# Kernel tuning notes

Hardware: AMD Instinct MI355X
Metric: run time of the kernel (lower is better)

Reference implementation:

```python
import jax, jax.numpy as jnp
import numpy as np

N, M, NTYPES, C, AXIS = 4096, 128, 2, 64, 16
TYPE_IDX = (0, 2048, 4096)        # atom-type partition along center axis
NTYPE_IDX = (0, 64, 128)          # neighbor-type partition along neighbor axis
RCUT = 6.0
BOX = 20.0
SR_MEAN = (0.1, 0.1)              # precomputed stats (get_stats)
SR_STD = (0.05, 0.05)
NORM = 20.0                       # avg neighbor count + 1


def setup_inputs() -> dict:
    key = jax.random.key(0)
    ks = jax.random.split(key, 16)
    coord_3N = jax.random.uniform(ks[0], (3, N), dtype=jnp.float32) * BOX
    box = jnp.full((3,), BOX, dtype=jnp.float32)
    # neighbors sorted by type: first 64 of type 0, last 64 of type 1
    nbr0 = jax.random.randint(ks[1], (N, M // 2), 0, TYPE_IDX[1])
    nbr1 = jax.random.randint(ks[2], (N, M // 2), TYPE_IDX[1], TYPE_IDX[2])
    nbrs_idx = jnp.concatenate([nbr0, nbr1], axis=1).astype(jnp.int32)
    # 4 per-(center,neighbor)-type embedding nets, widths 1->16->32->64, stacked
    eW0 = jax.random.normal(ks[3], (4, 1, 16), dtype=jnp.float32)
    eb0 = jax.random.normal(ks[4], (4, 16), dtype=jnp.float32) * 0.1
    eW1 = jax.random.normal(ks[5], (4, 16, 32), dtype=jnp.float32) / 4.0
    eb1 = jax.random.normal(ks[6], (4, 32), dtype=jnp.float32) * 0.1
    eW2 = jax.random.normal(ks[7], (4, 32, 64), dtype=jnp.float32) / (32.0 ** 0.5)
    eb2 = jax.random.normal(ks[8], (4, 64), dtype=jnp.float32) * 0.1
    Tbias = jnp.zeros((1, C), dtype=jnp.float32)
    # 2 per-type fitting nets, widths 1024->128->128->1, stacked
    fW0 = jax.random.normal(ks[9], (2, AXIS * C, 128), dtype=jnp.float32) / (AXIS * C) ** 0.5
    fb0 = jnp.zeros((2, 128), dtype=jnp.float32)
    fW1 = jax.random.normal(ks[10], (2, 128, 128), dtype=jnp.float32) / (128.0 ** 0.5)
    fb1 = jnp.zeros((2, 128), dtype=jnp.float32)
    fW2 = jax.random.normal(ks[11], (2, 128, 1), dtype=jnp.float32) / (128.0 ** 0.5)
    fb2 = jnp.zeros((2, 1), dtype=jnp.float32)
    Ebias = jnp.zeros((2,), dtype=jnp.float32)
    return {"coord_3N": coord_3N, "box": box, "nbrs_idx": nbrs_idx,
            "eW0": eW0, "eb0": eb0, "eW1": eW1, "eb1": eb1, "eW2": eW2, "eb2": eb2,
            "Tbias": Tbias, "fW0": fW0, "fb0": fb0, "fW1": fW1, "fb1": fb1,
            "fW2": fW2, "fb2": fb2, "Ebias": Ebias}


def reference(coord_3N, box, nbrs_idx, eW0, eb0, eW1, eb1, eW2, eb2,
              Tbias, fW0, fb0, fW1, fb1, fW2, fb2, Ebias):
    # --- neighbor gather + minimal-image relative coords (get_relative_coord) ---
    x_3NM = coord_3N[:, nbrs_idx] - coord_3N[:, :, None]            # [3,N,M]
    x_3NM = x_3NM - box[:, None, None] * jnp.round(x_3NM / box[:, None, None])
    r2 = (x_3NM ** 2).sum(0)
    mask = r2 > 1e-12
    rsafe = jnp.sqrt(jnp.where(mask, r2, 1.0))                      # safe for grads
    r_NM = jnp.where(mask, rsafe, 0.0)                              # [N,M]
    # --- smooth radial feature sr(r) = switch(r)/r ---
    sw = 0.5 * jnp.cos(jnp.pi * jnp.minimum(r_NM, RCUT) / RCUT) + 0.5
    sr_NM = jnp.where(mask & (r_NM < RCUT), sw / rsafe, 0.0)
    # --- per-center-type normalization (slice_t / concat_t over type_idx) ---
    srn_rows, srcn = [], []
    for i in range(NTYPES):
        blk = sr_NM[TYPE_IDX[i]:TYPE_IDX[i + 1]]
        srn_rows.append(blk / SR_STD[i])
        srcn.append((blk - SR_MEAN[i]) / SR_STD[i])
    sr_norm_NM = jnp.concatenate(srn_rows, 0)
    x_norm_3NM = x_3NM / jnp.where(mask, rsafe, 1.0)[None]
    R_3NM = 3 ** 0.5 * sr_norm_NM * x_norm_3NM
    R2diag_3NM = 9 ** 0.5 * sr_norm_NM * (x_norm_3NM ** 2 - 1.0 / 3.0)
    R2offd_3NM = 18 ** 0.5 * sr_norm_NM * (x_norm_3NM * jnp.stack([x_norm_3NM[1], x_norm_3NM[2], x_norm_3NM[0]]))
    R_XNM = jnp.concatenate([sr_norm_NM[None], R_3NM, R2diag_3NM, R2offd_3NM])  # [10,N,M]

    # --- per-(center,neighbor)-type embedding MLPs on scalar sr feature ---
    def embed(x, k):  # x: [n, m] -> [n, m, C]
        h = jnp.tanh(x[:, :, None] @ eW0[k] + eb0[k])
        h = jnp.tanh(h @ eW1[k] + eb1[k])
        return jnp.tanh(h @ eW2[k] + eb2[k])

    rows = []
    for i in range(NTYPES):
        cols = [embed(srcn[i][:, NTYPE_IDX[j]:NTYPE_IDX[j + 1]], i * NTYPES + j)
                for j in range(NTYPES)]
        rows.append(jnp.concatenate(cols, 1))
    embed_NMC = jnp.concatenate(rows, 0)                            # [N,M,C]

    # --- descriptor contraction ---
    T_NXC = jnp.einsum('xnm,nmc->nxc', R_XNM, embed_NMC) / NORM     # [N,10,C]
    T_NC = T_NXC[:, 0] + Tbias
    T_N3C = T_NXC[:, 1:4]
    T_N6C = T_NXC[:, 4:]
    G_NAC = T_NC[:, None] * T_NC[:, :AXIS, None] \
        + (T_N3C[:, :, None] * T_N3C[:, :, :AXIS, None]).sum(1)     # [N,AXIS,C]
    # use_2nd branch
    G1 = T_N3C[:, :, AXIS:2 * AXIS]                                 # [N,3,AXIS]
    G11 = jnp.concatenate([G1 ** 2,
                           2 ** 0.5 * G1 * jnp.stack([G1[:, 1], G1[:, 2], G1[:, 0]], axis=1)], axis=1)
    G2 = G11 + T_N6C[:, :, AXIS:2 * AXIS]                           # [N,6,AXIS]
    G_NAC = G_NAC + jnp.einsum('nxa,nxc->nac', G2, T_N6C)

    # --- per-type fitting nets ---
    Gflat = G_NAC.reshape(N, AXIS * C)
    energy = jnp.zeros((), dtype=Gflat.dtype)
    for t in range(NTYPES):
        g = Gflat[TYPE_IDX[t]:TYPE_IDX[t + 1]]
        h = jnp.tanh(g @ fW0[t] + fb0[t])
        h = jnp.tanh(h @ fW1[t] + fb1[t])
        f = h @ fW2[t] + fb2[t]
        energy = energy + (f + Ebias[t]).sum()
    return energy
```

## Files before the change

### kernel.cpp

```cpp
#include <hip/hip_runtime.h>
#include <hip/hip_fp16.h>

typedef _Float16 h16;
typedef h16 v2h __attribute__((ext_vector_type(2)));
typedef h16 v4h __attribute__((ext_vector_type(4)));
typedef h16 v8h __attribute__((ext_vector_type(8)));
typedef float f4 __attribute__((ext_vector_type(4)));

#define NATOM 4096
#define HALF_N 2048
#define K2 2.885390081777927f
#define GSCL 0.015625f
#define W0SCL (64.0f * K2)
#define USCL 0.0625f
#define GOUTS (GSCL / USCL)

#define TBL_N 2048
#define W0MIN_ (-0.201f)
#define DW_ (1.2005f / 2047.0f)
#define RSCALE_ (2047.0f / 1.2005f)

__device__ __forceinline__ float rcp_fast(float x) {
#if __has_builtin(__builtin_amdgcn_rcpf)
  return __builtin_amdgcn_rcpf(x);
#else
  return 1.0f / x;
#endif
}

__device__ __forceinline__ float exp2_fast(float x) {
#if __has_builtin(__builtin_amdgcn_exp2f)
  return __builtin_amdgcn_exp2f(x);
#else
  return exp2f(x);
#endif
}

__device__ __forceinline__ float tanh_e2(float d) {
  float r = rcp_fast(1.0f + exp2_fast(d));
  return fmaf(-2.0f, r, 1.0f);
}

__device__ __forceinline__ v8h lds_v8h(const h16* base, int byte) {
  return *(const v8h*)((const char*)base + byte);
}

__global__ __launch_bounds__(256) void k_setup(
    const float* __restrict__ eW0, const float* __restrict__ eb0,
    const float* __restrict__ eW1, const float* __restrict__ eb1,
    const float* __restrict__ eW2, const float* __restrict__ eb2,
    const float* __restrict__ fW0, const float* __restrict__ fW1,
    const float* __restrict__ coord,
    h16* __restrict__ tbl, h16* __restrict__ W0t, h16* __restrict__ W1t,
    f4* __restrict__ coordP)
{
  const int bid = blockIdx.x, tid = threadIdx.x;
  if (bid < 512) {
    __shared__ float sW1[512];
    __shared__ float sW2[2048];
    __shared__ float sW0s[16], sb0s[16], sb1s[32], sb2s[64];
    const int net = bid >> 7;
    for (int i = tid; i < 512; i += 256) sW1[i] = eW1[net * 512 + i];
    for (int i = tid; i < 2048; i += 256) sW2[i] = eW2[net * 2048 + i];
    if (tid < 16) { sW0s[tid] = eW0[net * 16 + tid]; sb0s[tid] = eb0[net * 16 + tid]; }
    else if (tid >= 32 && tid < 64) sb1s[tid - 32] = eb1[net * 32 + tid - 32];
    else if (tid >= 64 && tid < 128) sb2s[tid - 64] = eb2[net * 64 + tid - 64];
    __syncthreads();

    const int u = (bid & 127) * 256 + tid;
    const int e = u >> 4, cq = u & 15;
    const float w = W0MIN_ + (float)e * DW_;
    const float s = 8.0f * w * rcp_fast(1.0f - fabsf(w));
    float h0[16];
#pragma unroll
    for (int i = 0; i < 16; ++i)
      h0[i] = tanh_e2(K2 * fmaf(s, sW0s[i], sb0s[i]));
    float h1[32];
#pragma unroll
    for (int j = 0; j < 32; ++j) {
      float a = sb1s[j];
#pragma unroll
      for (int i = 0; i < 16; ++i) a = fmaf(h0[i], sW1[i * 32 + j], a);
      h1[j] = tanh_e2(K2 * a);
    }
    f4 a4 = *(const f4*)&sb2s[cq * 4];
    for (int j = 0; j < 32; ++j) {
      f4 wv4 = *(const f4*)&sW2[j * 64 + cq * 4];
      a4 += h1[j] * wv4;
    }
    union { h16 e4[4]; unsigned long long q; } o;
#pragma unroll
    for (int q = 0; q < 4; ++q) o.e4[q] = (h16)tanh_e2(K2 * a4[q]);
    *(unsigned long long*)&tbl[((size_t)(net * TBL_N + e)) * 64 + cq * 4] = o.q;
  } else if (bid < 640) {
    int idx = (bid - 512) * 256 + tid;
    int t = idx >> 14, n = idx & 127, k8 = (idx >> 7) & 127;
    union { v8h v; h16 e[8]; } o;
#pragma unroll
    for (int i = 0; i < 8; ++i)
      o.e[i] = (h16)(W0SCL * fW0[(size_t)t * 131072 + (size_t)(k8 * 8 + i) * 128 + n]);
    *(v8h*)&W0t[((size_t)t * 128 + n) * 1024 + k8 * 8] = o.v;
  } else if (bid < 656) {
    int idx = (bid - 640) * 256 + tid;
    f4 c;
    c.x = coord[idx]; c.y = coord[NATOM + idx]; c.z = coord[2 * NATOM + idx];
    c.w = 0.0f;
    coordP[idx] = c;
  } else {
    int idx = (bid - 656) * 256 + tid;
    int t = idx >> 11, rem = idx & 2047;
    int n = rem >> 4, k8 = rem & 15;
    union { v8h v; h16 e[8]; } o;
#pragma unroll
    for (int i = 0; i < 8; ++i)
      o.e[i] = (h16)(K2 * fW1[(size_t)t * 16384 + (size_t)(k8 * 8 + i) * 128 + n]);
    *(v8h*)&W1t[((size_t)t * 128 + n) * 128 + k8 * 8] = o.v;
  }
}

__global__ __launch_bounds__(256, 4) void k_embed(
    const f4* __restrict__ coordP, const float* __restrict__ box,
    const int* __restrict__ nbrs, const float* __restrict__ Tbias,
    const h16* __restrict__ tbl, h16* __restrict__ Gout)
{
  __shared__ h16 pool1[4][2560] __attribute__((aligned(16)));
  __shared__ h16 pool2[4][1360] __attribute__((aligned(16)));

  const int tid = threadIdx.x;
  const int wv = tid >> 6;
  const int lane = tid & 63;
  const int n = blockIdx.x * 4 + wv;
  const int ti = (n >= HALF_N) ? 1 : 0;
  const int c15 = lane & 15, g4 = lane >> 4;
  const int mp = lane >> 2, cg = lane & 3;

  h16* E32 = &pool1[wv][0];
  h16* Rl  = &pool2[wv][0];

  const int jnb0 = nbrs[(size_t)n * 128 + lane];
  const int jnb1 = nbrs[(size_t)n * 128 + 64 + lane];

  int uf0 = 0, uf1 = 0;
  {
    const float bx = box[0], by = box[1], bz = box[2];
    const float rbx = rcp_fast(bx), rby = rcp_fast(by), rbz = rcp_fast(bz);
    const f4 cme = coordP[n];
#pragma unroll
    for (int nb = 0; nb < 2; ++nb) {
      const int m = nb * 64 + lane;
      const f4 cj = coordP[nb ? jnb1 : jnb0];
      float dx = cj.x - cme.x;
      float dy = cj.y - cme.y;
      float dz = cj.z - cme.z;
      dx -= bx * rintf(dx * rbx);
      dy -= by * rintf(dy * rby);
      dz -= bz * rintf(dz * rbz);
      float r2 = dx * dx + dy * dy + dz * dz;
      bool mk = r2 > 1e-12f;
      float rs = sqrtf(mk ? r2 : 1.0f);
      float r  = mk ? rs : 0.0f;
      float sw = 0.5f * __cosf(0.52359878f * fminf(r, 6.0f)) + 0.5f;
      float invr = mk ? rcp_fast(rs) : 1.0f;
      float sr = (mk && r < 6.0f) ? sw * invr : 0.0f;
      float x0 = dx * invr, x1 = dy * invr, x2 = dz * invr;
      float srn = sr * 20.0f;
      float s   = (sr - 0.1f) * 20.0f;
      Rl[0 * 136 + m] = (h16)srn;
      Rl[1 * 136 + m] = (h16)(1.7320508f * srn * x0);
      Rl[2 * 136 + m] = (h16)(1.7320508f * srn * x1);
      Rl[3 * 136 + m] = (h16)(1.7320508f * srn * x2);
      Rl[4 * 136 + m] = (h16)(3.0f * srn * (x0 * x0 - 0.33333334f));
      Rl[5 * 136 + m] = (h16)(3.0f * srn * (x1 * x1 - 0.33333334f));
      Rl[6 * 136 + m] = (h16)(3.0f * srn * (x2 * x2 - 0.33333334f));
      Rl[7 * 136 + m] = (h16)(4.2426407f * srn * (x0 * x1));
      Rl[8 * 136 + m] = (h16)(4.2426407f * srn * (x1 * x2));
      Rl[9 * 136 + m] = (h16)(4.2426407f * srn * (x2 * x0));
      float wr = s * rcp_fast(8.0f + fabsf(s));
      float fidx = (wr - W0MIN_) * RSCALE_;
      fidx = fminf(fmaxf(fidx, 0.0f), 2045.99f);
      float i0f = floorf(fidx);
      h16 frh = (h16)(fidx - i0f);
      int uf = ((int)i0f << 16) |
               (int)__builtin_bit_cast(unsigned short, frh);
      if (nb == 0) uf0 = uf; else uf1 = uf;
    }
  }

  union U8 { v8h v; v2h p[4]; h16 e[8]; };
  const int rrow = (c15 < 10) ? c15 : 9;
  const v8h vzero = {};
  f4 tac[4];
#pragma unroll
  for (int nt = 0; nt < 4; ++nt) tac[nt] = (f4){0.f, 0.f, 0.f, 0.f};

  auto issue = [&](int ks, U8* buf, float* fr) {
#pragma unroll
    for (int e = 0; e < 2; ++e) {
      int src = ((ks & 1) * 32 + mp * 2 + e) * 4;
      unsigned uu = (unsigned)__builtin_amdgcn_ds_bpermute(src, (ks < 2) ? uf0 : uf1);
      int i0 = (int)(uu >> 16);
      fr[e] = (float)__builtin_bit_cast(h16, (unsigned short)(uu & 0xffffu));
      const int net = ti * 2 + (ks >> 1);
      const h16* rp = tbl + ((size_t)net * TBL_N + i0) * 64 + cg * 16;
      buf[e * 4 + 0].v = *(const v8h*)(rp);
      buf[e * 4 + 1].v = *(const v8h*)(rp + 8);
      buf[e * 4 + 2].v = *(const v8h*)(rp + 64);
      buf[e * 4 + 3].v = *(const v8h*)(rp + 72);
    }
  };

  auto proc = [&](int ks, U8* buf, const float* fr) {
    v2h f0; f0.x = (h16)fr[0]; f0.y = (h16)fr[0];
    v2h f1; f1.x = (h16)fr[1]; f1.y = (h16)fr[1];
    const int m0 = mp * 2;
#pragma unroll
    for (int ch8 = 0; ch8 < 2; ++ch8) {
#pragma unroll
      for (int p = 0; p < 4; ++p) {
        v2h e0 = buf[ch8].p[p]     + f0 * (buf[2 + ch8].p[p] - buf[ch8].p[p]);
        v2h e1 = buf[4 + ch8].p[p] + f1 * (buf[6 + ch8].p[p] - buf[4 + ch8].p[p]);
        const int c = cg * 16 + ch8 * 8 + p * 2;
        v2h w0; w0.x = e0.x; w0.y = e1.x;
        v2h w1; w1.x = e0.y; w1.y = e1.y;
        *(v2h*)&E32[c * 40 + m0]       = w0;
        *(v2h*)&E32[(c + 1) * 40 + m0] = w1;
      }
    }
    v8h ra = *(const v8h*)&Rl[rrow * 136 + ks * 32 + g4 * 8];
    if (c15 >= 10) ra = vzero;
#pragma unroll
    for (int nt = 0; nt < 4; ++nt) {
      v8h bf = *(const v8h*)&E32[(nt * 16 + c15) * 40 + g4 * 8];
      tac[nt] = __builtin_amdgcn_mfma_f32_16x16x32_f16(ra, bf, tac[nt], 0, 0, 0);
    }
  };

  U8 bA[8], bB[8];
  float frA[2], frB[2];
  issue(0, bA, frA);
  issue(1, bB, frB);
  proc(0, bA, frA);
  issue(2, bA, frA);
  proc(1, bB, frB);
  issue(3, bB, frB);
  proc(2, bA, frA);
  proc(3, bB, frB);

  h16* Vt = E32;
  h16* Ul = Rl;
#pragma unroll
  for (int nt = 0; nt < 4; ++nt) {
    const int col = nt * 16 + c15;
    float tb = (g4 == 0) ? Tbias[col] : 0.0f;
    v4h pk;
    pk[0] = (h16)(tac[nt][0] * 0.05f + tb);
    pk[1] = (h16)(tac[nt][1] * 0.05f);
    pk[2] = (h16)(tac[nt][2] * 0.05f);
    pk[3] = (h16)(tac[nt][3] * 0.05f);
    *(v4h*)&Vt[col * 40 + g4 * 4] = pk;
  }
  *(v8h*)&Vt[lane * 40 + 16] = vzero;
  *(v8h*)&Vt[lane * 40 + 24] = vzero;

  if (lane < 16) {
    const h16* va = &Vt[lane * 40];
    const h16* vb = &Vt[(16 + lane) * 40];
    v8h Ta = *(const v8h*)va;
    v8h Tb = *(const v8h*)vb;
    v2h Tb8 = *(const v2h*)(vb + 8);
    float g1x = (float)Tb[1], g1y = (float)Tb[2], g1z = (float)Tb[3];
    v8h up;
    up[0] = (h16)((float)Ta[0] * USCL);
    up[1] = (h16)((float)Ta[1] * USCL);
    up[2] = (h16)((float)Ta[2] * USCL);
    up[3] = (h16)((float)Ta[3] * USCL);
    up[4] = (h16)((g1x * g1x + (float)Tb[4]) * USCL);
    up[5] = (h16)((g1y * g1y + (float)Tb[5]) * USCL);
    up[6] = (h16)((g1z * g1z + (float)Tb[6]) * USCL);
    up[7] = (h16)((1.4142135f * g1x * g1y + (float)Tb[7]) * USCL);
    *(v8h*)&Ul[lane * 40] = up;
    v2h u89;
    u89.x = (h16)((1.4142135f * g1y * g1z + (float)Tb8[0]) * USCL);
    u89.y = (h16)((1.4142135f * g1z * g1x + (float)Tb8[1]) * USCL);
    *(v2h*)&Ul[lane * 40 + 8] = u89;
    v2h z2 = {};
    v4h z4 = {};
    *(v2h*)&Ul[lane * 40 + 10] = z2;
    *(v4h*)&Ul[lane * 40 + 12] = z4;
    *(v8h*)&Ul[lane * 40 + 16] = vzero;
    *(v8h*)&Ul[lane * 40 + 24] = vzero;
  }

  {
    v8h ua = *(const v8h*)&Ul[c15 * 40 + g4 * 8];
    h16* gp = Gout + (size_t)n * 1024;
#pragma unroll
    for (int nt = 0; nt < 4; ++nt) {
      v8h vb = *(const v8h*)&Vt[(nt * 16 + c15) * 40 + g4 * 8];
      f4 z = (f4){0.f, 0.f, 0.f, 0.f};
      f4 g = __builtin_amdgcn_mfma_f32_16x16x32_f16(ua, vb, z, 0, 0, 0);
#pragma unroll
      for (int r = 0; r < 4; ++r) {
        const int a = g4 * 4 + r;
        gp[a * 64 + nt * 16 + c15] = (h16)(g[r] * GOUTS);
      }
    }
  }
}

__global__ __launch_bounds__(256) void k_fit(
    const h16* __restrict__ G16, const h16* __restrict__ W0t,
    const h16* __restrict__ W1t,
    const float* __restrict__ fb0, const float* __restrict__ fb1,
    const float* __restrict__ fW2, const float* __restrict__ fb2,
    const float* __restrict__ Ebias, float* __restrict__ BP)
{
  __shared__ h16 As[2][32][64]  __attribute__((aligned(16)));
  __shared__ h16 Bs[2][128][64] __attribute__((aligned(16)));
  __shared__ h16 ht[32][128]    __attribute__((aligned(16)));
  __shared__ h16 W1s[128][128]  __attribute__((aligned(16)));
  __shared__ float red[32][33];

  const int tid = threadIdx.x;
  const int abase = blockIdx.x * 32;
  const int t = (abase >= HALF_N) ? 1 : 0;
  const int lane = tid & 63, w = tid >> 6;
  const int c15 = lane & 15, g4 = lane >> 4;
  const int rt = w & 1, ng = w >> 1;

  float fb0v[4], b1v[4], w2v[4];
#pragma unroll
  for (int nt = 0; nt < 4; ++nt) {
    const int nn = ng * 64 + nt * 16 + c15;
    fb0v[nt] = K2 * fb0[t * 128 + nn];
    b1v[nt]  = K2 * fb1[t * 128 + nn];
    w2v[nt]  = fW2[t * 128 + nn];
  }

#pragma unroll
  for (int u = 0; u < 8; ++u) {
    int idx = u * 256 + tid;
    int nrow = idx >> 4, c8 = idx & 15;
    v8h v = *(const v8h*)&W1t[((size_t)t * 128 + nrow) * 128 + c8 * 8];
    int byte = nrow * 256 + ((c8 * 16) ^ ((nrow & 7) << 4));
    *(v8h*)((char*)&W1s[0][0] + byte) = v;
  }

  f4 acc[4];
#pragma unroll
  for (int nt = 0; nt < 4; ++nt) acc[nt] = (f4){0.f, 0.f, 0.f, 0.f};

  auto stageK = [&](int kc, int p) {
    {
      int r = tid >> 3, c8 = tid & 7;
      v8h v = *(const v8h*)&G16[(size_t)(abase + r) * 1024 + kc * 64 + c8 * 8];
      int byte = r * 128 + ((c8 * 16) ^ ((r & 7) << 4));
      *(v8h*)((char*)&As[p][0][0] + byte) = v;
    }
#pragma unroll
    for (int u = 0; u < 4; ++u) {
      int idx = u * 256 + tid;
      int nrow = idx >> 3, c8 = idx & 7;
      v8h v = *(const v8h*)&W0t[((size_t)t * 128 + nrow) * 1024 + kc * 64 + c8 * 8];
      int byte = nrow * 128 + ((c8 * 16) ^ ((nrow & 7) << 4));
      *(v8h*)((char*)&Bs[p][0][0] + byte) = v;
    }
  };

  stageK(0, 0);
  __syncthreads();
  for (int kc = 0; kc < 16; ++kc) {
    const int p = kc & 1;
    if (kc < 15) stageK(kc + 1, p ^ 1);
#pragma unroll
    for (int ksub = 0; ksub < 2; ++ksub) {
      const int ar = rt * 16 + c15;
      const int koff = (ksub * 32 + g4 * 8) * 2;
      v8h a = lds_v8h(&As[p][0][0], ar * 128 + (koff ^ ((ar & 7) << 4)));
#pragma unroll
      for (int nt = 0; nt < 4; ++nt) {
        const int br = ng * 64 + nt * 16 + c15;
        v8h b = lds_v8h(&Bs[p][0][0], br * 128 + (koff ^ ((br & 7) << 4)));
        acc[nt] = __builtin_amdgcn_mfma_f32_16x16x32_f16(a, b, acc[nt], 0, 0, 0);
      }
    }
    __syncthreads();
  }

#pragma unroll
  for (int nt = 0; nt < 4; ++nt)
#pragma unroll
    for (int r = 0; r < 4; ++r) {
      int a = rt * 16 + g4 * 4 + r;
      int k = ng * 64 + nt * 16 + c15;
      h16 hv = (h16)tanh_e2(acc[nt][r] + fb0v[nt]);
      int byte = a * 256 + ((k * 2) ^ ((a & 7) << 4));
      *((h16*)((char*)&ht[0][0] + byte)) = hv;
    }
  __syncthreads();

  f4 acc2[4];
#pragma unroll
  for (int nt = 0; nt < 4; ++nt) acc2[nt] = (f4){0.f, 0.f, 0.f, 0.f};
#pragma unroll
  for (int ks2 = 0; ks2 < 4; ++ks2) {
    const int ar = rt * 16 + c15;
    const int koff = (ks2 * 32 + g4 * 8) * 2;
    v8h a = lds_v8h(&ht[0][0], ar * 256 + (koff ^ ((ar & 7) << 4)));
#pragma unroll
    for (int nt = 0; nt < 4; ++nt) {
      const int br = ng * 64 + nt * 16 + c15;
      v8h b = lds_v8h(&W1s[0][0], br * 256 + (koff ^ ((br & 7) << 4)));
      acc2[nt] = __builtin_amdgcn_mfma_f32_16x16x32_f16(a, b, acc2[nt], 0, 0, 0);
    }
  }

#pragma unroll
  for (int r = 0; r < 4; ++r) {
    float v = 0.0f;
#pragma unroll
    for (int nt = 0; nt < 4; ++nt)
      v += tanh_e2(acc2[nt][r] + b1v[nt]) * w2v[nt];
    red[rt * 16 + g4 * 4 + r][ng * 16 + c15] = v;
  }
  __syncthreads();
  if (tid < 64) {
    const int a = tid & 31, half = tid >> 5;
    float s = 0.0f;
#pragma unroll
    for (int c = 0; c < 16; ++c) s += red[a][half * 16 + c];
    s += __shfl_xor(s, 32);
    s += __shfl_xor(s, 16);
    s += __shfl_xor(s, 8);
    s += __shfl_xor(s, 4);
    s += __shfl_xor(s, 2);
    s += __shfl_xor(s, 1);
    if (tid == 0) BP[blockIdx.x] = s + 32.0f * (fb2[t] + Ebias[t]);
  }
}

__global__ __launch_bounds__(64) void k_reduce(const float* __restrict__ BP,
                                               float* __restrict__ out)
{
  int tid = threadIdx.x;
  float s = BP[tid] + BP[tid + 64];
  s += __shfl_xor(s, 32);
  s += __shfl_xor(s, 16);
  s += __shfl_xor(s, 8);
  s += __shfl_xor(s, 4);
  s += __shfl_xor(s, 2);
  s += __shfl_xor(s, 1);
  if (tid == 0) out[0] = s;
}

extern "C" void kernel_launch(void* const* d_in, const int* in_sizes, int n_in,
                              void* d_out, int out_size, void* d_ws, size_t ws_size,
                              hipStream_t stream) {
  const float* coord = (const float*)d_in[0];
  const float* box   = (const float*)d_in[1];
  const int*   nbrs  = (const int*)d_in[2];
  const float* eW0   = (const float*)d_in[3];
  const float* eb0   = (const float*)d_in[4];
  const float* eW1   = (const float*)d_in[5];
  const float* eb1   = (const float*)d_in[6];
  const float* eW2   = (const float*)d_in[7];
  const float* eb2   = (const float*)d_in[8];
  const float* Tbias = (const float*)d_in[9];
  const float* fW0   = (const float*)d_in[10];
  const float* fb0   = (const float*)d_in[11];
  const float* fW1   = (const float*)d_in[12];
  const float* fb1   = (const float*)d_in[13];
  const float* fW2   = (const float*)d_in[14];
  const float* fb2   = (const float*)d_in[15];
  const float* Ebias = (const float*)d_in[16];

  char* ws = (char*)d_ws;
  h16*   G16 = (h16*)ws;
  h16*   W0t = (h16*)(ws + (size_t)8  * 1024 * 1024);
  h16*   W1t = (h16*)(ws + (size_t)9  * 1024 * 1024);
  h16*   tbl = (h16*)(ws + (size_t)10 * 1024 * 1024);
  f4*    cP  = (f4*)(ws + (size_t)11 * 1024 * 1024);
  float* BP  = (float*)(ws + (size_t)12 * 1024 * 1024);

  k_setup<<<672, 256, 0, stream>>>(eW0, eb0, eW1, eb1, eW2, eb2, fW0, fW1,
                                   coord, tbl, W0t, W1t, cP);
  k_embed<<<1024, 256, 0, stream>>>(cP, box, nbrs, Tbias, tbl, G16);
  k_fit<<<128, 256, 0, stream>>>(G16, W0t, W1t, fb0, fb1, fW2, fb2, Ebias, BP);
  k_reduce<<<1, 64, 0, stream>>>(BP, (float*)d_out);
}
```

Baseline: 42.70 us.

## Halve fit tile rows, double blocks, fuse final reduction via atomic counter

The fitting kernel now processes 16 atoms per block instead of 32, launching 256 blocks to fill more compute units, with a larger K-chunk and a single shared LDS pool reused across stages. The separate reduction kernel is removed: each block publishes its partial sum and the last block to arrive, detected via an atomic counter reset in setup, sums all partials. The setup embedding layer-1 matmul is also vectorised using a transposed weight layout. This trades duplicate weight loads per block and atomic ordering overhead for better occupancy and one fewer launch.

```diff
diff --git a/kernel.cpp b/kernel.cpp
--- a/kernel.cpp
+++ b/kernel.cpp
@@ -52,15 +52,18 @@
     const float* __restrict__ fW0, const float* __restrict__ fW1,
     const float* __restrict__ coord,
     h16* __restrict__ tbl, h16* __restrict__ W0t, h16* __restrict__ W1t,
-    f4* __restrict__ coordP)
+    f4* __restrict__ coordP, int* __restrict__ counter)
 {
   const int bid = blockIdx.x, tid = threadIdx.x;
   if (bid < 512) {
-    __shared__ float sW1[512];
+    __shared__ float sW1t[32][16];
     __shared__ float sW2[2048];
     __shared__ float sW0s[16], sb0s[16], sb1s[32], sb2s[64];
     const int net = bid >> 7;
-    for (int i = tid; i < 512; i += 256) sW1[i] = eW1[net * 512 + i];
+    for (int i = tid; i < 512; i += 256) {
+      int j = i >> 4, ii = i & 15;
+      sW1t[j][ii] = eW1[net * 512 + ii * 32 + j];
+    }
     for (int i = tid; i < 2048; i += 256) sW2[i] = eW2[net * 2048 + i];
     if (tid < 16) { sW0s[tid] = eW0[net * 16 + tid]; sb0s[tid] = eb0[net * 16 + tid]; }
     else if (tid >= 32 && tid < 64) sb1s[tid - 32] = eb1[net * 32 + tid - 32];
@@ -75,12 +78,20 @@
 #pragma unroll
     for (int i = 0; i < 16; ++i)
       h0[i] = tanh_e2(K2 * fmaf(s, sW0s[i], sb0s[i]));
+    f4 h04[4];
+#pragma unroll
+    for (int q = 0; q < 4; ++q) {
+      h04[q].x = h0[q * 4]; h04[q].y = h0[q * 4 + 1];
+      h04[q].z = h0[q * 4 + 2]; h04[q].w = h0[q * 4 + 3];
+    }
     float h1[32];
 #pragma unroll
     for (int j = 0; j < 32; ++j) {
-      float a = sb1s[j];
-#pragma unroll
-      for (int i = 0; i < 16; ++i) a = fmaf(h0[i], sW1[i * 32 + j], a);
+      f4 p = h04[0] * (*(const f4*)&sW1t[j][0]);
+      p += h04[1] * (*(const f4*)&sW1t[j][4]);
+      p += h04[2] * (*(const f4*)&sW1t[j][8]);
+      p += h04[3] * (*(const f4*)&sW1t[j][12]);
+      float a = sb1s[j] + (p.x + p.y) + (p.z + p.w);
       h1[j] = tanh_e2(K2 * a);
     }
     f4 a4 = *(const f4*)&sb2s[cq * 4];
@@ -101,6 +112,7 @@
       o.e[i] = (h16)(W0SCL * fW0[(size_t)t * 131072 + (size_t)(k8 * 8 + i) * 128 + n]);
     *(v8h*)&W0t[((size_t)t * 128 + n) * 1024 + k8 * 8] = o.v;
   } else if (bid < 656) {
+    if (bid == 640 && tid == 0) *counter = 0;
     int idx = (bid - 640) * 256 + tid;
     f4 c;
     c.x = coord[idx]; c.y = coord[NATOM + idx]; c.z = coord[2 * NATOM + idx];
@@ -308,149 +320,152 @@
   }
 }
 
-__global__ __launch_bounds__(256) void k_fit(
+__global__ __launch_bounds__(256, 2) void k_fit(
     const h16* __restrict__ G16, const h16* __restrict__ W0t,
     const h16* __restrict__ W1t,
     const float* __restrict__ fb0, const float* __restrict__ fb1,
     const float* __restrict__ fW2, const float* __restrict__ fb2,
-    const float* __restrict__ Ebias, float* __restrict__ BP)
+    const float* __restrict__ Ebias,
+    float* __restrict__ BP, int* __restrict__ counter,
+    float* __restrict__ out)
 {
-  __shared__ h16 As[2][32][64]  __attribute__((aligned(16)));
-  __shared__ h16 Bs[2][128][64] __attribute__((aligned(16)));
-  __shared__ h16 ht[32][128]    __attribute__((aligned(16)));
-  __shared__ h16 W1s[128][128]  __attribute__((aligned(16)));
-  __shared__ float red[32][33];
-
+  __shared__ h16 pool[36864] __attribute__((aligned(16)));
+  __shared__ int lastFlag;
   const int tid = threadIdx.x;
-  const int abase = blockIdx.x * 32;
+  const int abase = blockIdx.x * 16;
   const int t = (abase >= HALF_N) ? 1 : 0;
   const int lane = tid & 63, w = tid >> 6;
   const int c15 = lane & 15, g4 = lane >> 4;
-  const int rt = w & 1, ng = w >> 1;
-
-  float fb0v[4], b1v[4], w2v[4];
-#pragma unroll
-  for (int nt = 0; nt < 4; ++nt) {
-    const int nn = ng * 64 + nt * 16 + c15;
+
+  float fb0v[2], b1v[2], w2v[2];
+#pragma unroll
+  for (int nt = 0; nt < 2; ++nt) {
+    const int nn = w * 32 + nt * 16 + c15;
     fb0v[nt] = K2 * fb0[t * 128 + nn];
     b1v[nt]  = K2 * fb1[t * 128 + nn];
     w2v[nt]  = fW2[t * 128 + nn];
   }
 
+  auto stageK = [&](int kc, int p) {
+    {
+      int r = tid >> 4, c8 = tid & 15;
+      v8h v = *(const v8h*)&G16[(size_t)(abase + r) * 1024 + kc * 128 + c8 * 8];
+      int byte = p * 36864 + r * 256 + ((c8 * 16) ^ ((r & 7) << 4));
+      *(v8h*)((char*)pool + byte) = v;
+    }
+#pragma unroll
+    for (int u = 0; u < 8; ++u) {
+      int idx = u * 256 + tid;
+      int nr = idx >> 4, c8 = idx & 15;
+      v8h v = *(const v8h*)&W0t[((size_t)t * 128 + nr) * 1024 + kc * 128 + c8 * 8];
+      int byte = p * 36864 + 4096 + nr * 256 + ((c8 * 16) ^ ((nr & 7) << 4));
+      *(v8h*)((char*)pool + byte) = v;
+    }
+  };
+
+  f4 acc[2];
+  acc[0] = (f4){0.f, 0.f, 0.f, 0.f};
+  acc[1] = (f4){0.f, 0.f, 0.f, 0.f};
+
+  stageK(0, 0);
+  __syncthreads();
+  for (int kc = 0; kc < 8; ++kc) {
+    const int p = kc & 1;
+    if (kc < 7) stageK(kc + 1, p ^ 1);
+#pragma unroll
+    for (int ksub = 0; ksub < 4; ++ksub) {
+      const int koff = (ksub * 32 + g4 * 8) * 2;
+      v8h a = lds_v8h(pool, p * 36864 + c15 * 256 + (koff ^ ((c15 & 7) << 4)));
+#pragma unroll
+      for (int nt = 0; nt < 2; ++nt) {
+        const int br = w * 32 + nt * 16 + c15;
+        v8h b = lds_v8h(pool,
+                        p * 36864 + 4096 + br * 256 + (koff ^ ((br & 7) << 4)));
+        acc[nt] = __builtin_amdgcn_mfma_f32_16x16x32_f16(a, b, acc[nt], 0, 0, 0);
+      }
+    }
+    __syncthreads();
+  }
+
+#pragma unroll
+  for (int nt = 0; nt < 2; ++nt)
+#pragma unroll
+    for (int r = 0; r < 4; ++r) {
+      int a = g4 * 4 + r;
+      int col = w * 32 + nt * 16 + c15;
+      h16 hv = (h16)tanh_e2(acc[nt][r] + fb0v[nt]);
+      int byte = a * 256 + ((col * 2) ^ ((a & 7) << 4));
+      *((h16*)((char*)pool + byte)) = hv;
+    }
 #pragma unroll
   for (int u = 0; u < 8; ++u) {
     int idx = u * 256 + tid;
-    int nrow = idx >> 4, c8 = idx & 15;
-    v8h v = *(const v8h*)&W1t[((size_t)t * 128 + nrow) * 128 + c8 * 8];
-    int byte = nrow * 256 + ((c8 * 16) ^ ((nrow & 7) << 4));
-    *(v8h*)((char*)&W1s[0][0] + byte) = v;
-  }
-
-  f4 acc[4];
-#pragma unroll
-  for (int nt = 0; nt < 4; ++nt) acc[nt] = (f4){0.f, 0.f, 0.f, 0.f};
-
-  auto stageK = [&](int kc, int p) {
-    {
-      int r = tid >> 3, c8 = tid & 7;
-      v8h v = *(const v8h*)&G16[(size_t)(abase + r) * 1024 + kc * 64 + c8 * 8];
-      int byte = r * 128 + ((c8 * 16) ^ ((r & 7) << 4));
-      *(v8h*)((char*)&As[p][0][0] + byte) = v;
-    }
-#pragma unroll
-    for (int u = 0; u < 4; ++u) {
-      int idx = u * 256 + tid;
-      int nrow = idx >> 3, c8 = idx & 7;
-      v8h v = *(const v8h*)&W0t[((size_t)t * 128 + nrow) * 1024 + kc * 64 + c8 * 8];
-      int byte = nrow * 128 + ((c8 * 16) ^ ((nrow & 7) << 4));
-      *(v8h*)((char*)&Bs[p][0][0] + byte) = v;
-    }
-  };
-
-  stageK(0, 0);
+    int nr = idx >> 4, c8 = idx & 15;
+    v8h v = *(const v8h*)&W1t[((size_t)t * 128 + nr) * 128 + c8 * 8];
+    int byte = 4096 + nr * 256 + ((c8 * 16) ^ ((nr & 7) << 4));
+    *(v8h*)((char*)pool + byte) = v;
+  }
   __syncthreads();
-  for (int kc = 0; kc < 16; ++kc) {
-    const int p = kc & 1;
-    if (kc < 15) stageK(kc + 1, p ^ 1);
-#pragma unroll
-    for (int ksub = 0; ksub < 2; ++ksub) {
-      const int ar = rt * 16 + c15;
-      const int koff = (ksub * 32 + g4 * 8) * 2;
-      v8h a = lds_v8h(&As[p][0][0], ar * 128 + (koff ^ ((ar & 7) << 4)));
-#pragma unroll
-      for (int nt = 0; nt < 4; ++nt) {
-        const int br = ng * 64 + nt * 16 + c15;
-        v8h b = lds_v8h(&Bs[p][0][0], br * 128 + (koff ^ ((br & 7) << 4)));
-        acc[nt] = __builtin_amdgcn_mfma_f32_16x16x32_f16(a, b, acc[nt], 0, 0, 0);
-      }
-    }
-    __syncthreads();
-  }
-
-#pragma unroll
-  for (int nt = 0; nt < 4; ++nt)
-#pragma unroll
-    for (int r = 0; r < 4; ++r) {
-      int a = rt * 16 + g4 * 4 + r;
-      int k = ng * 64 + nt * 16 + c15;
-      h16 hv = (h16)tanh_e2(acc[nt][r] + fb0v[nt]);
-      int byte = a * 256 + ((k * 2) ^ ((a & 7) << 4));
-      *((h16*)((char*)&ht[0][0] + byte)) = hv;
-    }
-  __syncthreads();
-
-  f4 acc2[4];
-#pragma unroll
-  for (int nt = 0; nt < 4; ++nt) acc2[nt] = (f4){0.f, 0.f, 0.f, 0.f};
+
+  f4 acc2[2];
+  acc2[0] = (f4){0.f, 0.f, 0.f, 0.f};
+  acc2[1] = (f4){0.f, 0.f, 0.f, 0.f};
 #pragma unroll
   for (int ks2 = 0; ks2 < 4; ++ks2) {
-    const int ar = rt * 16 + c15;
     const int koff = (ks2 * 32 + g4 * 8) * 2;
-    v8h a = lds_v8h(&ht[0][0], ar * 256 + (koff ^ ((ar & 7) << 4)));
-#pragma unroll
-    for (int nt = 0; nt < 4; ++nt) {
-      const int br = ng * 64 + nt * 16 + c15;
-      v8h b = lds_v8h(&W1s[0][0], br * 256 + (koff ^ ((br & 7) << 4)));
+    v8h a = lds_v8h(pool, c15 * 256 + (koff ^ ((c15 & 7) << 4)));
+#pragma unroll
+    for (int nt = 0; nt < 2; ++nt) {
+      const int br = w * 32 + nt * 16 + c15;
+      v8h b = lds_v8h(pool, 4096 + br * 256 + (koff ^ ((br & 7) << 4)));
       acc2[nt] = __builtin_amdgcn_mfma_f32_16x16x32_f16(a, b, acc2[nt], 0, 0, 0);
     }
   }
 
+  float* redp = (float*)((char*)pool + 40960);
 #pragma unroll
   for (int r = 0; r < 4; ++r) {
     float v = 0.0f;
 #pragma unroll
-    for (int nt = 0; nt < 4; ++nt)
+    for (int nt = 0; nt < 2; ++nt)
       v += tanh_e2(acc2[nt][r] + b1v[nt]) * w2v[nt];
-    red[rt * 16 + g4 * 4 + r][ng * 16 + c15] = v;
+    redp[(g4 * 4 + r) * 64 + w * 16 + c15] = v;
   }
   __syncthreads();
   if (tid < 64) {
-    const int a = tid & 31, half = tid >> 5;
     float s = 0.0f;
 #pragma unroll
-    for (int c = 0; c < 16; ++c) s += red[a][half * 16 + c];
+    for (int u = 0; u < 16; ++u) s += redp[tid + u * 64];
     s += __shfl_xor(s, 32);
     s += __shfl_xor(s, 16);
     s += __shfl_xor(s, 8);
     s += __shfl_xor(s, 4);
     s += __shfl_xor(s, 2);
     s += __shfl_xor(s, 1);
-    if (tid == 0) BP[blockIdx.x] = s + 32.0f * (fb2[t] + Ebias[t]);
-  }
-}
-
-__global__ __launch_bounds__(64) void k_reduce(const float* __restrict__ BP,
-                                               float* __restrict__ out)
-{
-  int tid = threadIdx.x;
-  float s = BP[tid] + BP[tid + 64];
-  s += __shfl_xor(s, 32);
-  s += __shfl_xor(s, 16);
-  s += __shfl_xor(s, 8);
-  s += __shfl_xor(s, 4);
-  s += __shfl_xor(s, 2);
-  s += __shfl_xor(s, 1);
-  if (tid == 0) out[0] = s;
+    if (tid == 0) {
+      float blockSum = s + 16.0f * (fb2[t] + Ebias[t]);
+      __hip_atomic_store(&BP[blockIdx.x], blockSum, __ATOMIC_RELEASE,
+                         __HIP_MEMORY_SCOPE_AGENT);
+      int old = __hip_atomic_fetch_add(counter, 1, __ATOMIC_ACQ_REL,
+                                       __HIP_MEMORY_SCOPE_AGENT);
+      lastFlag = (old == 255) ? 1 : 0;
+    }
+  }
+  __syncthreads();
+  if (lastFlag && tid < 64) {
+    float s = 0.0f;
+#pragma unroll
+    for (int q = 0; q < 4; ++q)
+      s += __hip_atomic_load(&BP[tid + q * 64], __ATOMIC_ACQUIRE,
+                             __HIP_MEMORY_SCOPE_AGENT);
+    s += __shfl_xor(s, 32);
+    s += __shfl_xor(s, 16);
+    s += __shfl_xor(s, 8);
+    s += __shfl_xor(s, 4);
+    s += __shfl_xor(s, 2);
+    s += __shfl_xor(s, 1);
+    if (tid == 0) out[0] = s;
+  }
 }
 
 extern "C" void kernel_launch(void* const* d_in, const int* in_sizes, int n_in,
@@ -481,10 +496,11 @@
   h16*   tbl = (h16*)(ws + (size_t)10 * 1024 * 1024);
   f4*    cP  = (f4*)(ws + (size_t)11 * 1024 * 1024);
   float* BP  = (float*)(ws + (size_t)12 * 1024 * 1024);
+  int*   cnt = (int*)(ws + (size_t)12 * 1024 * 1024 + 4096);
 
   k_setup<<<672, 256, 0, stream>>>(eW0, eb0, eW1, eb1, eW2, eb2, fW0, fW1,
-                                   coord, tbl, W0t, W1t, cP);
+                                   coord, tbl, W0t, W1t, cP, cnt);
   k_embed<<<1024, 256, 0, stream>>>(cP, box, nbrs, Tbias, tbl, G16);
-  k_fit<<<128, 256, 0, stream>>>(G16, W0t, W1t, fb0, fb1, fW2, fb2, Ebias, BP);
-  k_reduce<<<1, 64, 0, stream>>>(BP, (float*)d_out);
-}
+  k_fit<<<256, 256, 0, stream>>>(G16, W0t, W1t, fb0, fb1, fW2, fb2, Ebias,
+                                 BP, cnt, (float*)d_out);
+}
```

Result: slower. 45.46 us (+6.5%).
